# Kernel optimization log

Measured on AMD Instinct MI355X. Metric: run time of the kernel, lower is better.

## Reference

```python
import jax, jax.numpy as jnp
import numpy as np

B, T, D = 16, 32, 4096
H, HD = 32, 128          # n_heads, head_dim
MAX_SEQ = 2048
START_POS = 1024


def _rope(x):
    # x: [b, t, h, hd]; faithful to source: positions start at 0 (no start_pos offset)
    t, hd = x.shape[1], x.shape[-1]
    theta = 10000.0 ** (-2.0 * jnp.arange(0, hd, 2, dtype=jnp.float32) / hd)  # [hd/2]
    freqs = jnp.arange(t, dtype=jnp.float32)[:, None] * theta                 # [t, hd/2]
    cos = jnp.repeat(jnp.cos(freqs), 2, axis=-1)[None, :, None, :]            # [1,t,1,hd]
    sin = jnp.repeat(jnp.sin(freqs), 2, axis=-1)[None, :, None, :]
    # rotate: even slots <- -odd, odd slots <- even (interleaved)
    x_rot = jnp.stack([-x[..., 1::2], x[..., 0::2]], axis=-1).reshape(x.shape)
    return x * cos + x_rot * sin


def setup_inputs() -> dict:
    key = jax.random.key(0)
    ks = jax.random.split(key, 7)
    s = 0.02
    return {
        "x": jax.random.normal(ks[0], (B, T, D), dtype=jnp.float32),
        "wq": jax.random.normal(ks[1], (D, D), dtype=jnp.float32) * s,
        "wk": jax.random.normal(ks[2], (D, D), dtype=jnp.float32) * s,
        "wv": jax.random.normal(ks[3], (D, D), dtype=jnp.float32) * s,
        "wo": jax.random.normal(ks[4], (D, D), dtype=jnp.float32) * s,
        "k_cache": jax.random.normal(ks[5], (B, MAX_SEQ, H, HD), dtype=jnp.float32),
        "v_cache": jax.random.normal(ks[6], (B, MAX_SEQ, H, HD), dtype=jnp.float32),
        "start_pos": START_POS,
    }


def reference(x, wq, wk, wv, wo, k_cache, v_cache, start_pos):
    b, t, _ = x.shape
    xq = (x @ wq).reshape(b, t, H, HD)
    xk = (x @ wk).reshape(b, t, H, HD)
    xv = (x @ wv).reshape(b, t, H, HD)
    xq = _rope(xq)
    xk = _rope(xk)
    # KV-cache append (start_pos is a static Python int)
    k_cache = jax.lax.dynamic_update_slice(k_cache, xk, (0, start_pos, 0, 0))
    v_cache = jax.lax.dynamic_update_slice(v_cache, xv, (0, start_pos, 0, 0))
    L = start_pos + t
    keys = k_cache[:, :L]    # [b, L, h, hd]
    values = v_cache[:, :L]
    # n_rep == 1 -> repeat_kv is identity
    scores = jnp.einsum("bthd,bshd->bhts", xq, keys) / np.float32(np.sqrt(HD))
    probs = jax.nn.softmax(scores.astype(jnp.float32), axis=-1).astype(xq.dtype)
    out = jnp.einsum("bhts,bshd->bthd", probs, values).reshape(b, t, H * HD)
    return out @ wo
```

## Files before the change

kernel.cpp:

```cpp
#include <hip/hip_runtime.h>
#include <hip/hip_bf16.h>

#define B_ 16
#define T_ 32
#define D_ 4096
#define H_ 32
#define HD_ 128
#define MAXS_ 2048
#define M_ (B_*T_)

typedef __hip_bfloat16 bf16;
typedef __attribute__((ext_vector_type(8))) short bf16x8;
typedef __attribute__((ext_vector_type(4))) float f32x4;

static __device__ __forceinline__ short f2b(float f) {
    bf16 h = __float2bfloat16(f);
    return *reinterpret_cast<short*>(&h);
}
static __device__ __forceinline__ float b2f(short s) {
    bf16 h;
    *reinterpret_cast<short*>(&h) = s;
    return __bfloat162float(h);
}

#define GLD16(gsrc, ldst) \
    __builtin_amdgcn_global_load_lds((const __attribute__((address_space(1))) void*)(gsrc), \
        (__attribute__((address_space(3))) void*)(ldst), 16, 0, 0)

__global__ __launch_bounds__(256) void conv_x(const float* __restrict__ x, bf16* __restrict__ xb) {
    int idx = blockIdx.x * 256 + threadIdx.x;
    const float4* xf = (const float4*)x;
    float4 a = xf[idx * 2], b = xf[idx * 2 + 1];
    bf16x8 o;
    o[0] = f2b(a.x); o[1] = f2b(a.y); o[2] = f2b(a.z); o[3] = f2b(a.w);
    o[4] = f2b(b.x); o[5] = f2b(b.y); o[6] = f2b(b.z); o[7] = f2b(b.w);
    *(bf16x8*)&xb[(size_t)idx * 8] = o;
}

__global__ __launch_bounds__(256) void transpose_w(const float* __restrict__ W, bf16* __restrict__ wt) {
    __shared__ float Ts[64][65];
    const int n0 = blockIdx.x * 64, k0 = blockIdx.y * 64;
    const int t = threadIdx.x;
    {
        int kk = t >> 4, nn = (t & 15) * 4;
        #pragma unroll
        for (int r = 0; r < 4; ++r) {
            float4 v = *(const float4*)&W[(size_t)(k0 + kk + 16 * r) * D_ + n0 + nn];
            Ts[kk + 16 * r][nn + 0] = v.x;
            Ts[kk + 16 * r][nn + 1] = v.y;
            Ts[kk + 16 * r][nn + 2] = v.z;
            Ts[kk + 16 * r][nn + 3] = v.w;
        }
    }
    __syncthreads();
    const int kg = t & 7, nr = t >> 3;
    #pragma unroll
    for (int r = 0; r < 2; ++r) {
        int n = nr + 32 * r;
        bf16x8 o;
        #pragma unroll
        for (int j = 0; j < 8; ++j) o[j] = f2b(Ts[kg * 8 + j][n]);
        *(bf16x8*)&wt[(size_t)(n0 + n) * D_ + k0 + kg * 8] = o;
    }
}

__global__ __launch_bounds__(256) void gemm_qkvw(const bf16* __restrict__ A,
        const float* __restrict__ wq, const float* __restrict__ wk,
        const float* __restrict__ wv, bf16* __restrict__ out) {
    const int K = D_;
    const int wsel = blockIdx.x >> 5;
    const float* W = (wsel == 0) ? wq : (wsel == 1) ? wk : wv;
    const int lcol0 = (blockIdx.x & 31) * 128;
    bf16* Ob = out + (size_t)wsel * M_ * D_;
    __shared__ bf16 As[2][64 * 32];
    __shared__ short Bs[2][128][40];
    const int tid = threadIdx.x, lane = tid & 63, wave = tid >> 6;
    const int wr = wave >> 1, wc = wave & 1;
    const int lg = lane >> 4, li = lane & 15;
    const int row0 = blockIdx.y * 64;
    const int bq = tid & 31, kq = tid >> 5;
    f32x4 acc[2][4];
    #pragma unroll
    for (int i = 0; i < 2; ++i)
        #pragma unroll
        for (int j = 0; j < 4; ++j)
            #pragma unroll
            for (int r = 0; r < 4; ++r) acc[i][j][r] = 0.f;

    const int sw = (li & 3) << 4;
    for (int k0 = 0; k0 < K; k0 += 64) {
        float4 wv4[2][4];
        #pragma unroll
        for (int h = 0; h < 2; ++h)
            #pragma unroll
            for (int i = 0; i < 4; ++i)
                wv4[h][i] = *(const float4*)&W[(size_t)(k0 + 32 * h + kq * 4 + i) * D_ + lcol0 + bq * 4];
        {
            int X = tid * 16;
            int row = X >> 6;
            int kb = (X & 63) ^ ((row & 3) << 4);
            GLD16(A + (size_t)(row0 + row) * K + k0 + (kb >> 1),      (char*)As[0] + wave * 1024);
            GLD16(A + (size_t)(row0 + row) * K + k0 + 32 + (kb >> 1), (char*)As[1] + wave * 1024);
        }
        #pragma unroll
        for (int h = 0; h < 2; ++h)
            #pragma unroll
            for (int j = 0; j < 4; ++j) {
                int n = bq * 4 + j;
                short4 col;
                col.x = f2b(((const float*)&wv4[h][0])[j]);
                col.y = f2b(((const float*)&wv4[h][1])[j]);
                col.z = f2b(((const float*)&wv4[h][2])[j]);
                col.w = f2b(((const float*)&wv4[h][3])[j]);
                *(short4*)((char*)&Bs[h][n][0] + ((kq * 8) ^ (((n >> 4) & 3) << 4))) = col;
            }
        __syncthreads();
        bf16x8 af[2][2], bfr[2][4];
        #pragma unroll
        for (int h = 0; h < 2; ++h) {
            #pragma unroll
            for (int i = 0; i < 2; ++i) {
                int row = wr * 32 + i * 16 + li;
                af[h][i] = *(const bf16x8*)((const char*)As[h] + row * 64 + ((lg * 16) ^ sw));
            }
            #pragma unroll
            for (int j = 0; j < 4; ++j) {
                int row = wc * 64 + j * 16 + li;
                bfr[h][j] = *(const bf16x8*)((const char*)&Bs[h][row][0] + ((lg * 16) ^ (((row >> 4) & 3) << 4)));
            }
        }
        #pragma unroll
        for (int h = 0; h < 2; ++h)
            #pragma unroll
            for (int i = 0; i < 2; ++i)
                #pragma unroll
                for (int j = 0; j < 4; ++j)
                    acc[i][j] = __builtin_amdgcn_mfma_f32_16x16x32_bf16(af[h][i], bfr[h][j], acc[i][j], 0, 0, 0);
        __syncthreads();
    }
    #pragma unroll
    for (int i = 0; i < 2; ++i)
        for (int j = 0; j < 4; ++j)
            for (int r = 0; r < 4; ++r) {
                int row = row0 + wr * 32 + i * 16 + lg * 4 + r;
                int col = lcol0 + wc * 64 + j * 16 + li;
                Ob[(size_t)row * D_ + col] = __float2bfloat16(acc[i][j][r]);
            }
}

template<int BM, int BN>
__global__ __launch_bounds__(256) void gemm_bf16t(const bf16* __restrict__ A,
        const bf16* __restrict__ Bt, float* __restrict__ O) {
    constexpr int IM = BM / 32;
    constexpr int JN = BN / 32;
    constexpr int nA = (BM * 64) / 4096;
    constexpr int nB = (BN * 64) / 4096;
    const int K = D_;
    __shared__ bf16 As[2][BM * 32];
    __shared__ bf16 Bs[2][BN * 32];
    const int tid = threadIdx.x, lane = tid & 63, wave = tid >> 6;
    const int wr = wave >> 1, wc = wave & 1;
    const int lg = lane >> 4, li = lane & 15;
    const int row0 = blockIdx.y * BM, col0 = blockIdx.x * BN;
    f32x4 acc[IM][JN];
    #pragma unroll
    for (int i = 0; i < IM; ++i)
        #pragma unroll
        for (int j = 0; j < JN; ++j)
            #pragma unroll
            for (int r = 0; r < 4; ++r) acc[i][j][r] = 0.f;

    const int sw = (li & 3) << 4;
    for (int k0 = 0; k0 < K; k0 += 64) {
        #pragma unroll
        for (int h = 0; h < 2; ++h) {
            #pragma unroll
            for (int i = 0; i < nA; ++i) {
                int X = (i * 256 + tid) * 16;
                int row = X >> 6;
                int kb = (X & 63) ^ ((row & 3) << 4);
                GLD16(A + (size_t)(row0 + row) * K + k0 + 32 * h + (kb >> 1),
                      (char*)As[h] + (i * 256 + wave * 64) * 16);
            }
            #pragma unroll
            for (int i = 0; i < nB; ++i) {
                int X = (i * 256 + tid) * 16;
                int row = X >> 6;
                int kb = (X & 63) ^ ((row & 3) << 4);
                GLD16(Bt + (size_t)(col0 + row) * K + k0 + 32 * h + (kb >> 1),
                      (char*)Bs[h] + (i * 256 + wave * 64) * 16);
            }
        }
        __syncthreads();
        bf16x8 af[2][IM], bfr[2][JN];
        #pragma unroll
        for (int h = 0; h < 2; ++h) {
            #pragma unroll
            for (int i = 0; i < IM; ++i) {
                int row = wr * (BM / 2) + i * 16 + li;
                af[h][i] = *(const bf16x8*)((const char*)As[h] + row * 64 + ((lg * 16) ^ sw));
            }
            #pragma unroll
            for (int j = 0; j < JN; ++j) {
                int row = wc * (BN / 2) + j * 16 + li;
                bfr[h][j] = *(const bf16x8*)((const char*)Bs[h] + row * 64 + ((lg * 16) ^ sw));
            }
        }
        #pragma unroll
        for (int h = 0; h < 2; ++h)
            #pragma unroll
            for (int i = 0; i < IM; ++i)
                #pragma unroll
                for (int j = 0; j < JN; ++j)
                    acc[i][j] = __builtin_amdgcn_mfma_f32_16x16x32_bf16(af[h][i], bfr[h][j], acc[i][j], 0, 0, 0);
        __syncthreads();
    }
    #pragma unroll
    for (int i = 0; i < IM; ++i)
        for (int j = 0; j < JN; ++j)
            for (int r = 0; r < 4; ++r) {
                int row = row0 + wr * (BM / 2) + i * 16 + lg * 4 + r;
                int col = col0 + wc * (BN / 2) + j * 16 + li;
                O[(size_t)row * D_ + col] = acc[i][j][r];
            }
}

__global__ __launch_bounds__(256) void rope_inplace(bf16* __restrict__ qb, bf16* __restrict__ kb) {
    int idx = blockIdx.x * 256 + threadIdx.x;
    size_t e0 = (size_t)idx * 8;
    int hd0 = (int)(e0 & 127);
    int t = (int)((e0 >> 12) & 31);
    bf16x8 q = *(bf16x8*)&qb[e0];
    bf16x8 k = *(bf16x8*)&kb[e0];
    bf16x8 qo, ko;
    #pragma unroll
    for (int p = 0; p < 4; ++p) {
        int i = (hd0 >> 1) + p;
        float theta = exp2f(-(float)i * 0.41524101186092787f);
        float s, c;
        sincosf((float)t * theta, &s, &c);
        float q0 = b2f(q[2 * p]), q1 = b2f(q[2 * p + 1]);
        qo[2 * p]     = f2b(q0 * c - q1 * s);
        qo[2 * p + 1] = f2b(q1 * c + q0 * s);
        float k0 = b2f(k[2 * p]), k1 = b2f(k[2 * p + 1]);
        ko[2 * p]     = f2b(k0 * c - k1 * s);
        ko[2 * p + 1] = f2b(k1 * c + k0 * s);
    }
    *(bf16x8*)&qb[e0] = qo;
    *(bf16x8*)&kb[e0] = ko;
}

__global__ __launch_bounds__(256, 2) void attn(const bf16* __restrict__ qb,
        const bf16* __restrict__ kb, const bf16* __restrict__ vb,
        const float* __restrict__ kc, const float* __restrict__ vc,
        const int* __restrict__ spp, bf16* __restrict__ ob) {
    const int bh = blockIdx.x;
    const int b = bh >> 5, h = bh & 31;
    const int sp = *spp;
    const int L = sp + T_;
    const int tid = threadIdx.x, lane = tid & 63, wave = tid >> 6;
    const int lg = lane >> 4, li = lane & 15;

    __shared__ __align__(16) char smem[76928];
    char* VLDSw = smem + wave * 16384;
    float(*Vf)[128] = (float(*)[128])VLDSw;
    auto Plds = (bf16(*)[32][40])(smem + 65536);
    auto msh  = (float(*)[32])(smem + 75776);
    auto lsh  = (float(*)[32])(smem + 76288);
    float* ltot = (float*)(smem + 76800);
    float(*Osh)[128] = (float(*)[128])smem;

    bf16x8 qf[2][4];
    #pragma unroll
    for (int rt = 0; rt < 2; ++rt)
        #pragma unroll
        for (int kk = 0; kk < 4; ++kk)
            qf[rt][kk] = *(const bf16x8*)(&qb[((size_t)(b * T_ + rt * 16 + li) * H_ + h) * HD_ + kk * 32 + lg * 8]);

    f32x4 o[2][8];
    float m_r[2], l_r[2];
    m_r[0] = m_r[1] = -1e30f;
    l_r[0] = l_r[1] = 0.f;
    #pragma unroll
    for (int rt = 0; rt < 2; ++rt) for (int ht = 0; ht < 8; ++ht) for (int r = 0; r < 4; ++r) o[rt][ht][r] = 0.f;

    const float scale = 0.08838834764831845f;
    const int nch = (L + 31) >> 5;
    const int ccache = sp >> 5;

    bf16x8 kf[2][4];
    float4 kr[16];

    auto KISSUE = [&](int cc) {
        #pragma unroll
        for (int ct = 0; ct < 2; ++ct) {
            const float* kp = &kc[(((size_t)b * MAXS_ + cc * 32 + ct * 16 + li) * H_ + h) * HD_ + lg * 8];
            #pragma unroll
            for (int kk = 0; kk < 4; ++kk) {
                kr[ct * 8 + 2 * kk]     = *(const float4*)(kp + kk * 32);
                kr[ct * 8 + 2 * kk + 1] = *(const float4*)(kp + kk * 32 + 4);
            }
        }
    };
    auto VSTAGE = [&](int cc) {
        const float* src = vc + (((size_t)b * MAXS_ + cc * 32) * H_ + h) * HD_;
        #pragma unroll
        for (int i = 0; i < 16; ++i) {
            GLD16(src + (size_t)(2 * i + (lane >> 5)) * (H_ * HD_) + (lane & 31) * 4,
                  VLDSw + i * 1024);
        }
    };
    auto KBUILD = [&]() {
        #pragma unroll
        for (int ct = 0; ct < 2; ++ct)
            #pragma unroll
            for (int kk = 0; kk < 4; ++kk) {
                bf16x8 f;
                f[0] = f2b(kr[ct * 8 + 2 * kk].x); f[1] = f2b(kr[ct * 8 + 2 * kk].y);
                f[2] = f2b(kr[ct * 8 + 2 * kk].z); f[3] = f2b(kr[ct * 8 + 2 * kk].w);
                f[4] = f2b(kr[ct * 8 + 2 * kk + 1].x); f[5] = f2b(kr[ct * 8 + 2 * kk + 1].y);
                f[6] = f2b(kr[ct * 8 + 2 * kk + 1].z); f[7] = f2b(kr[ct * 8 + 2 * kk + 1].w);
                kf[ct][kk] = f;
            }
    };

    auto COMPUTE = [&](int s0, bool deep) {
        f32x4 sc[2][2];
        #pragma unroll
        for (int ct = 0; ct < 2; ++ct)
            #pragma unroll
            for (int rt = 0; rt < 2; ++rt) {
                f32x4 acc;
                for (int r = 0; r < 4; ++r) acc[r] = 0.f;
                #pragma unroll
                for (int kk = 0; kk < 4; ++kk)
                    acc = __builtin_amdgcn_mfma_f32_16x16x32_bf16(kf[ct][kk], qf[rt][kk], acc, 0, 0, 0);
                sc[ct][rt] = acc;
            }
        float corr[2];
        #pragma unroll
        for (int rt = 0; rt < 2; ++rt) {
            float xv[8];
            #pragma unroll
            for (int ct = 0; ct < 2; ++ct)
                #pragma unroll
                for (int r = 0; r < 4; ++r) {
                    float xx = sc[ct][rt][r] * scale;
                    if (s0 + ct * 16 + 4 * lg + r >= L) xx = -1e30f;
                    xv[ct * 4 + r] = xx;
                }
            float mx = fmaxf(fmaxf(fmaxf(xv[0], xv[1]), fmaxf(xv[2], xv[3])),
                             fmaxf(fmaxf(xv[4], xv[5]), fmaxf(xv[6], xv[7])));
            mx = fmaxf(mx, __shfl_xor(mx, 16, 64));
            mx = fmaxf(mx, __shfl_xor(mx, 32, 64));
            float mnew = fmaxf(m_r[rt], mx);
            corr[rt] = __expf(m_r[rt] - mnew);
            float p[8], ssum = 0.f;
            #pragma unroll
            for (int j = 0; j < 8; ++j) { p[j] = __expf(xv[j] - mnew); ssum += p[j]; }
            ssum += __shfl_xor(ssum, 16, 64);
            ssum += __shfl_xor(ssum, 32, 64);
            l_r[rt] = l_r[rt] * corr[rt] + ssum;
            m_r[rt] = mnew;
            #pragma unroll
            for (int ct = 0; ct < 2; ++ct)
                #pragma unroll
                for (int r = 0; r < 4; ++r)
                    Plds[wave][rt * 16 + li][ct * 16 + 4 * lg + r] = __float2bfloat16(p[ct * 4 + r]);
        }
        #pragma unroll
        for (int rt = 0; rt < 2; ++rt) {
            float cq[4];
            #pragma unroll
            for (int r = 0; r < 4; ++r) cq[r] = __shfl(corr[rt], 20 * lg + r, 64);
            #pragma unroll
            for (int ht = 0; ht < 8; ++ht)
                #pragma unroll
                for (int r = 0; r < 4; ++r) o[rt][ht][r] *= cq[r];
        }
        if (deep) asm volatile("s_waitcnt vmcnt(16) lgkmcnt(0)" ::: "memory");
        else      asm volatile("s_waitcnt vmcnt(0) lgkmcnt(0)" ::: "memory");
        __builtin_amdgcn_sched_barrier(0);
        bf16x8 pf[2];
        pf[0] = *(const bf16x8*)(&Plds[wave][li][lg * 8]);
        pf[1] = *(const bf16x8*)(&Plds[wave][16 + li][lg * 8]);
        #pragma unroll
        for (int ht = 0; ht < 8; ++ht) {
            bf16x8 vf;
            #pragma unroll
            for (int j = 0; j < 8; ++j)
                vf[j] = f2b(Vf[lg * 8 + j][ht * 16 + li]);
            #pragma unroll
            for (int rt = 0; rt < 2; ++rt)
                o[rt][ht] = __builtin_amdgcn_mfma_f32_16x16x32_bf16(pf[rt], vf, o[rt][ht], 0, 0, 0);
        }
    };

    int c = wave;
    if (c < ccache) {
        KISSUE(c);
        VSTAGE(c);
        for (;;) {
            const int s0 = c * 32;
            const int nc = c + 4;
            const bool more = nc < ccache;
            KBUILD();
            if (more) KISSUE(nc);
            COMPUTE(s0, more);
            asm volatile("s_waitcnt lgkmcnt(0)" ::: "memory");
            if (more) VSTAGE(nc);
            c = nc;
            if (!more) break;
        }
    }
    for (; c < nch; c += 4) {
        const int s0 = c * 32;
        #pragma unroll
        for (int u = 0; u < 16; ++u) {
            int F = lane + 64 * u;
            int s = F >> 5, q = F & 31;
            int ss = s0 + s;
            float4 v;
            if (ss < sp) {
                v = *(const float4*)&vc[(((size_t)b * MAXS_ + ss) * H_ + h) * HD_ + q * 4];
            } else if (ss < L) {
                ushort4 uu = *(const ushort4*)&vb[(((size_t)b * T_ + (ss - sp)) * H_ + h) * HD_ + q * 4];
                v = make_float4(b2f((short)uu.x), b2f((short)uu.y), b2f((short)uu.z), b2f((short)uu.w));
            } else {
                v = make_float4(0.f, 0.f, 0.f, 0.f);
            }
            *(float4*)&Vf[s][q * 4] = v;
        }
        #pragma unroll
        for (int ct = 0; ct < 2; ++ct) {
            int s = s0 + ct * 16 + li;
            if (s < sp) {
                const float* kp = &kc[(((size_t)b * MAXS_ + s) * H_ + h) * HD_];
                #pragma unroll
                for (int kk = 0; kk < 4; ++kk) {
                    float4 v0 = *(const float4*)(&kp[kk * 32 + lg * 8]);
                    float4 v1 = *(const float4*)(&kp[kk * 32 + lg * 8 + 4]);
                    bf16x8 f;
                    f[0] = f2b(v0.x); f[1] = f2b(v0.y); f[2] = f2b(v0.z); f[3] = f2b(v0.w);
                    f[4] = f2b(v1.x); f[5] = f2b(v1.y); f[6] = f2b(v1.z); f[7] = f2b(v1.w);
                    kf[ct][kk] = f;
                }
            } else if (s < L) {
                const bf16* kp = &kb[((size_t)(b * T_ + s - sp) * H_ + h) * HD_];
                #pragma unroll
                for (int kk = 0; kk < 4; ++kk)
                    kf[ct][kk] = *(const bf16x8*)(kp + kk * 32 + lg * 8);
            } else {
                #pragma unroll
                for (int kk = 0; kk < 4; ++kk) {
                    bf16x8 f;
                    #pragma unroll
                    for (int j = 0; j < 8; ++j) f[j] = 0;
                    kf[ct][kk] = f;
                }
            }
        }
        COMPUTE(s0, false);
    }

    if (lg == 0) {
        #pragma unroll
        for (int rt = 0; rt < 2; ++rt) {
            msh[wave][rt * 16 + li] = m_r[rt];
            lsh[wave][rt * 16 + li] = l_r[rt];
        }
    }
    __syncthreads();
    float corr2[2][4];
    #pragma unroll
    for (int rt = 0; rt < 2; ++rt)
        for (int r = 0; r < 4; ++r) {
            int row = rt * 16 + lg * 4 + r;
            float M = fmaxf(fmaxf(msh[0][row], msh[1][row]), fmaxf(msh[2][row], msh[3][row]));
            corr2[rt][r] = __expf(msh[wave][row] - M);
        }
    if (tid < 32) {
        int row = tid;
        float M = fmaxf(fmaxf(msh[0][row], msh[1][row]), fmaxf(msh[2][row], msh[3][row]));
        float lt = 0.f;
        #pragma unroll
        for (int w = 0; w < 4; ++w) lt += lsh[w][row] * __expf(msh[w][row] - M);
        ltot[row] = lt;
    }
    __syncthreads();
    for (int w = 0; w < 4; ++w) {
        if (wave == w) {
            #pragma unroll
            for (int rt = 0; rt < 2; ++rt)
                for (int ht = 0; ht < 8; ++ht)
                    for (int r = 0; r < 4; ++r) {
                        int row = rt * 16 + lg * 4 + r, col = ht * 16 + li;
                        float val = o[rt][ht][r] * corr2[rt][r];
                        if (w == 0) Osh[row][col] = val;
                        else Osh[row][col] += val;
                    }
        }
        __syncthreads();
    }
    {
        int row = tid >> 3;
        int c0 = (tid & 7) * 16;
        float inv = 1.0f / ltot[row];
        #pragma unroll
        for (int j = 0; j < 16; ++j)
            ob[(size_t)(b * T_ + row) * D_ + h * HD_ + c0 + j] = __float2bfloat16(Osh[row][c0 + j] * inv);
    }
}

extern "C" void kernel_launch(void* const* d_in, const int* in_sizes, int n_in,
                              void* d_out, int out_size, void* d_ws, size_t ws_size,
                              hipStream_t stream) {
    const float* x  = (const float*)d_in[0];
    const float* wq = (const float*)d_in[1];
    const float* wk = (const float*)d_in[2];
    const float* wv = (const float*)d_in[3];
    const float* wo = (const float*)d_in[4];
    const float* kc = (const float*)d_in[5];
    const float* vc = (const float*)d_in[6];
    const int*   sp = (const int*)d_in[7];

    char* ws = (char*)d_ws;
    const size_t MT = (size_t)M_ * D_;
    bf16* wt = (bf16*)ws;
    bf16* xb = wt + (size_t)D_ * D_;
    bf16* qb = xb + MT;
    bf16* kb = qb + MT;
    bf16* vb = kb + MT;
    bf16* ab = vb + MT;

    conv_x<<<dim3((int)(MT / 8 / 256)), 256, 0, stream>>>(x, xb);
    transpose_w<<<dim3(64, 64), 256, 0, stream>>>(wo, wt);
    gemm_qkvw<<<dim3(96, 8), 256, 0, stream>>>(xb, wq, wk, wv, qb);
    rope_inplace<<<dim3((int)(MT / 8 / 256)), 256, 0, stream>>>(qb, kb);
    attn<<<dim3(B_ * H_), 256, 0, stream>>>(qb, kb, vb, kc, vc, sp, ab);
    gemm_bf16t<64, 64><<<dim3(64, 8), 256, 0, stream>>>(ab, wt, (float*)d_out);
}
```

Baseline: 318.2 us.

## Split-K the QKV projection and fuse partial reduction into RoPE kernel

The QKV GEMM is split into two K halves via a third grid dimension, each writing fp32 partial results to a new workspace buffer. The RoPE kernel becomes a combine kernel that sums the two partials, applies RoPE to q and k, and converts q, k and v to bf16. This doubles the block count to improve GPU occupancy, but adds substantial fp32 partial write and read traffic plus extra workspace.

```diff
diff --git a/kernel.cpp b/kernel.cpp
--- a/kernel.cpp
+++ b/kernel.cpp
@@ -66,12 +66,12 @@
 
 __global__ __launch_bounds__(256) void gemm_qkvw(const bf16* __restrict__ A,
         const float* __restrict__ wq, const float* __restrict__ wk,
-        const float* __restrict__ wv, bf16* __restrict__ out) {
-    const int K = D_;
+        const float* __restrict__ wv, float* __restrict__ P) {
     const int wsel = blockIdx.x >> 5;
     const float* W = (wsel == 0) ? wq : (wsel == 1) ? wk : wv;
     const int lcol0 = (blockIdx.x & 31) * 128;
-    bf16* Ob = out + (size_t)wsel * M_ * D_;
+    const int z = blockIdx.z;
+    float* Ob = P + (size_t)z * 3 * ((size_t)M_ * D_) + (size_t)wsel * M_ * D_;
     __shared__ bf16 As[2][64 * 32];
     __shared__ short Bs[2][128][40];
     const int tid = threadIdx.x, lane = tid & 63, wave = tid >> 6;
@@ -88,7 +88,8 @@
             for (int r = 0; r < 4; ++r) acc[i][j][r] = 0.f;
 
     const int sw = (li & 3) << 4;
-    for (int k0 = 0; k0 < K; k0 += 64) {
+    const int kbeg = z * (D_ / 2), kend = kbeg + (D_ / 2);
+    for (int k0 = kbeg; k0 < kend; k0 += 64) {
         float4 wv4[2][4];
         #pragma unroll
         for (int h = 0; h < 2; ++h)
@@ -99,8 +100,8 @@
             int X = tid * 16;
             int row = X >> 6;
             int kb = (X & 63) ^ ((row & 3) << 4);
-            GLD16(A + (size_t)(row0 + row) * K + k0 + (kb >> 1),      (char*)As[0] + wave * 1024);
-            GLD16(A + (size_t)(row0 + row) * K + k0 + 32 + (kb >> 1), (char*)As[1] + wave * 1024);
+            GLD16(A + (size_t)(row0 + row) * D_ + k0 + (kb >> 1),      (char*)As[0] + wave * 1024);
+            GLD16(A + (size_t)(row0 + row) * D_ + k0 + 32 + (kb >> 1), (char*)As[1] + wave * 1024);
         }
         #pragma unroll
         for (int h = 0; h < 2; ++h)
@@ -144,7 +145,7 @@
             for (int r = 0; r < 4; ++r) {
                 int row = row0 + wr * 32 + i * 16 + lg * 4 + r;
                 int col = lcol0 + wc * 64 + j * 16 + li;
-                Ob[(size_t)row * D_ + col] = __float2bfloat16(acc[i][j][r]);
+                Ob[(size_t)row * D_ + col] = acc[i][j][r];
             }
 }
 
@@ -225,29 +226,39 @@
             }
 }
 
-__global__ __launch_bounds__(256) void rope_inplace(bf16* __restrict__ qb, bf16* __restrict__ kb) {
+__global__ __launch_bounds__(256) void rope_combine(const float* __restrict__ P,
+        bf16* __restrict__ qb, bf16* __restrict__ kb, bf16* __restrict__ vb) {
+    const size_t MT = (size_t)M_ * D_;
     int idx = blockIdx.x * 256 + threadIdx.x;
     size_t e0 = (size_t)idx * 8;
-    int hd0 = (int)(e0 & 127);
-    int t = (int)((e0 >> 12) & 31);
-    bf16x8 q = *(bf16x8*)&qb[e0];
-    bf16x8 k = *(bf16x8*)&kb[e0];
-    bf16x8 qo, ko;
-    #pragma unroll
-    for (int p = 0; p < 4; ++p) {
-        int i = (hd0 >> 1) + p;
-        float theta = exp2f(-(float)i * 0.41524101186092787f);
-        float s, c;
-        sincosf((float)t * theta, &s, &c);
-        float q0 = b2f(q[2 * p]), q1 = b2f(q[2 * p + 1]);
-        qo[2 * p]     = f2b(q0 * c - q1 * s);
-        qo[2 * p + 1] = f2b(q1 * c + q0 * s);
-        float k0 = b2f(k[2 * p]), k1 = b2f(k[2 * p + 1]);
-        ko[2 * p]     = f2b(k0 * c - k1 * s);
-        ko[2 * p + 1] = f2b(k1 * c + k0 * s);
-    }
-    *(bf16x8*)&qb[e0] = qo;
-    *(bf16x8*)&kb[e0] = ko;
+    int t3 = (int)(e0 >> 21);
+    size_t e = e0 & (MT - 1);
+    const float4* p0 = (const float4*)P;
+    const float4* p1 = (const float4*)(P + 3 * MT);
+    float4 a = p0[idx * 2], b = p0[idx * 2 + 1];
+    float4 c = p1[idx * 2], d = p1[idx * 2 + 1];
+    float v8[8] = { a.x + c.x, a.y + c.y, a.z + c.z, a.w + c.w,
+                    b.x + d.x, b.y + d.y, b.z + d.z, b.w + d.w };
+    bf16x8 o;
+    if (t3 < 2) {
+        int hd0 = (int)(e & 127);
+        int tp = (int)((e >> 12) & 31);
+        #pragma unroll
+        for (int p = 0; p < 4; ++p) {
+            int i = (hd0 >> 1) + p;
+            float theta = exp2f(-(float)i * 0.41524101186092787f);
+            float s, cc;
+            sincosf((float)tp * theta, &s, &cc);
+            float x0 = v8[2 * p], x1 = v8[2 * p + 1];
+            o[2 * p]     = f2b(x0 * cc - x1 * s);
+            o[2 * p + 1] = f2b(x1 * cc + x0 * s);
+        }
+    } else {
+        #pragma unroll
+        for (int j = 0; j < 8; ++j) o[j] = f2b(v8[j]);
+    }
+    bf16* dst = (t3 == 0) ? qb : (t3 == 1) ? kb : vb;
+    *(bf16x8*)&dst[e] = o;
 }
 
 __global__ __launch_bounds__(256, 2) void attn(const bf16* __restrict__ qb,
@@ -532,11 +543,12 @@
     bf16* kb = qb + MT;
     bf16* vb = kb + MT;
     bf16* ab = vb + MT;
+    float* Pf = (float*)(ab + MT);
 
     conv_x<<<dim3((int)(MT / 8 / 256)), 256, 0, stream>>>(x, xb);
     transpose_w<<<dim3(64, 64), 256, 0, stream>>>(wo, wt);
-    gemm_qkvw<<<dim3(96, 8), 256, 0, stream>>>(xb, wq, wk, wv, qb);
-    rope_inplace<<<dim3((int)(MT / 8 / 256)), 256, 0, stream>>>(qb, kb);
+    gemm_qkvw<<<dim3(96, 8, 2), 256, 0, stream>>>(xb, wq, wk, wv, Pf);
+    rope_combine<<<dim3((int)(3 * MT / 8 / 256)), 256, 0, stream>>>(Pf, qb, kb, vb);
     attn<<<dim3(B_ * H_), 256, 0, stream>>>(qb, kb, vb, kc, vc, sp, ab);
     gemm_bf16t<64, 64><<<dim3(64, 8), 256, 0, stream>>>(ab, wt, (float*)d_out);
 }
```

New measurement: 332.6 us. +4.5%, slower.

## Register-prefetch next K tile in projection GEMM to overlap loads with MFMA

Applied to the files above, without the earlier changes.

Restructures the fp32-weight projection GEMM main loop into a two-stage register double-buffer. The next K-slice of W and A is loaded into registers while MFMAs run on the current tile, and the A tile now goes through registers instead of a direct global-to-LDS load. This aims to hide global memory latency behind compute, at the cost of more registers (two sets of float4 W buffers), which could reduce occupancy. The loop now assumes K is a multiple of 128.

```diff
diff --git a/kernel.cpp b/kernel.cpp
--- a/kernel.cpp
+++ b/kernel.cpp
@@ -88,33 +88,38 @@
             for (int r = 0; r < 4; ++r) acc[i][j][r] = 0.f;
 
     const int sw = (li & 3) << 4;
-    for (int k0 = 0; k0 < K; k0 += 64) {
-        float4 wv4[2][4];
+    const int Arow = tid >> 2;
+    const int Akb = ((tid * 16) & 63) ^ ((Arow & 3) << 4);
+    const char* Abase = (const char*)(A + (size_t)(row0 + Arow) * K) + Akb;
+
+    auto WLOAD = [&](int k0, float4 (&wvv)[2][4]) {
         #pragma unroll
         for (int h = 0; h < 2; ++h)
             #pragma unroll
             for (int i = 0; i < 4; ++i)
-                wv4[h][i] = *(const float4*)&W[(size_t)(k0 + 32 * h + kq * 4 + i) * D_ + lcol0 + bq * 4];
-        {
-            int X = tid * 16;
-            int row = X >> 6;
-            int kb = (X & 63) ^ ((row & 3) << 4);
-            GLD16(A + (size_t)(row0 + row) * K + k0 + (kb >> 1),      (char*)As[0] + wave * 1024);
-            GLD16(A + (size_t)(row0 + row) * K + k0 + 32 + (kb >> 1), (char*)As[1] + wave * 1024);
-        }
+                wvv[h][i] = *(const float4*)&W[(size_t)(k0 + 32 * h + kq * 4 + i) * D_ + lcol0 + bq * 4];
+    };
+    auto ALOAD = [&](int k0, uint4 (&avv)[2]) {
+        avv[0] = *(const uint4*)(Abase + (size_t)k0 * 2);
+        avv[1] = *(const uint4*)(Abase + (size_t)k0 * 2 + 64);
+    };
+    auto STAGE = [&](float4 (&wvv)[2][4], uint4 (&avv)[2]) {
+        *(uint4*)((char*)As[0] + tid * 16) = avv[0];
+        *(uint4*)((char*)As[1] + tid * 16) = avv[1];
         #pragma unroll
         for (int h = 0; h < 2; ++h)
             #pragma unroll
             for (int j = 0; j < 4; ++j) {
                 int n = bq * 4 + j;
                 short4 col;
-                col.x = f2b(((const float*)&wv4[h][0])[j]);
-                col.y = f2b(((const float*)&wv4[h][1])[j]);
-                col.z = f2b(((const float*)&wv4[h][2])[j]);
-                col.w = f2b(((const float*)&wv4[h][3])[j]);
+                col.x = f2b(((const float*)&wvv[h][0])[j]);
+                col.y = f2b(((const float*)&wvv[h][1])[j]);
+                col.z = f2b(((const float*)&wvv[h][2])[j]);
+                col.w = f2b(((const float*)&wvv[h][3])[j]);
                 *(short4*)((char*)&Bs[h][n][0] + ((kq * 8) ^ (((n >> 4) & 3) << 4))) = col;
             }
-        __syncthreads();
+    };
+    auto STEP = [&]() {
         bf16x8 af[2][2], bfr[2][4];
         #pragma unroll
         for (int h = 0; h < 2; ++h) {
@@ -136,6 +141,26 @@
                 #pragma unroll
                 for (int j = 0; j < 4; ++j)
                     acc[i][j] = __builtin_amdgcn_mfma_f32_16x16x32_bf16(af[h][i], bfr[h][j], acc[i][j], 0, 0, 0);
+    };
+
+    float4 wA[2][4], wB[2][4];
+    uint4 aA[2], aB[2];
+    WLOAD(0, wA);
+    ALOAD(0, aA);
+    for (int k0 = 0; k0 < K; k0 += 128) {
+        STAGE(wA, aA);
+        WLOAD(k0 + 64, wB);
+        ALOAD(k0 + 64, aB);
+        __syncthreads();
+        STEP();
+        __syncthreads();
+        STAGE(wB, aB);
+        if (k0 + 128 < K) {
+            WLOAD(k0 + 128, wA);
+            ALOAD(k0 + 128, aA);
+        }
+        __syncthreads();
+        STEP();
         __syncthreads();
     }
     #pragma unroll
```

Result: slower. 424.2 us (+33.3%).
